# Performance work log

Measured on AMD Instinct MI355X. Metric: run time of the kernel, lower is better.

The kernel has to match this reference:

```python
import jax, jax.numpy as jnp
import numpy as np

N = 50000      # nodes
E = 800000     # edges
IN = 128       # in_feats
NH = 128       # n_hidden (per-head out_feats)
H = 2          # num_heads
P = 100000     # node pairs for the head MLP
C = 2          # n_classes
NEG_SLOPE = 0.2


def setup_inputs() -> dict:
    key = jax.random.key(0)
    ks = jax.random.split(key, 16)
    def glorot(k, shape, fan_in):
        return jax.random.normal(k, shape, jnp.float32) * (1.0 / np.sqrt(fan_in))
    return {
        "src": jax.random.randint(ks[0], (E,), 0, N),
        "dst": jax.random.randint(ks[1], (E,), 0, N),
        "h": jax.random.normal(ks[2], (N, IN), jnp.float32),
        "x1": jax.random.randint(ks[3], (P,), 0, N),
        "x2": jax.random.randint(ks[4], (P,), 0, N),
        # GATConv layer 0
        "W0": glorot(ks[5], (IN, H * NH), IN),
        "al0": glorot(ks[6], (H, NH), NH),
        "ar0": glorot(ks[7], (H, NH), NH),
        # GATConv layer 1
        "W1": glorot(ks[8], (NH, H * NH), NH),
        "al1": glorot(ks[9], (H, NH), NH),
        "ar1": glorot(ks[10], (H, NH), NH),
        # head MLP (weights stored as [in, out])
        "w1": glorot(ks[11], (3 * NH, NH), 3 * NH),
        "b1": jnp.zeros((NH,), jnp.float32),
        "w2": glorot(ks[12], (NH, C), NH),
        "b2": jnp.zeros((C,), jnp.float32),
    }


def gat_conv(h, src, dst, W, al, ar):
    # h: [N, d_in] -> feat: [N, H, F]
    feat = (h @ W).reshape(h.shape[0], H, -1)
    el = jnp.einsum("nhf,hf->nh", feat, al)  # [N, H]
    er = jnp.einsum("nhf,hf->nh", feat, ar)  # [N, H]
    e = jax.nn.leaky_relu(el[src] + er[dst], NEG_SLOPE)  # [E, H]
    # edge softmax segmented by destination node
    emax = jax.ops.segment_max(e, dst, num_segments=N)
    ee = jnp.exp(e - emax[dst])
    denom = jax.ops.segment_sum(ee, dst, num_segments=N)
    alpha = ee / (denom[dst] + 1e-9)                      # [E, H]
    msg = feat[src] * alpha[..., None]                    # [E, H, F]
    out = jax.ops.segment_sum(msg, dst, num_segments=N)   # [N, H, F]
    return jax.nn.relu(out)


def reference(src, dst, h, x1, x2, W0, al0, ar0, W1, al1, ar1, w1, b1, w2, b2):
    h = gat_conv(h, src, dst, W0, al0, ar0).mean(axis=1)  # [N, NH]
    h = gat_conv(h, src, dst, W1, al1, ar1).mean(axis=1)  # [N, NH]
    h1, h2 = h[x1], h[x2]                                 # [P, NH]
    z = jnp.concatenate([h1, h2, jnp.abs(h1 - h2)], axis=1)
    z = jax.nn.relu(z @ w1 + b1)
    return z @ w2 + b2                                    # [P, C]
```

## Files before the change

kernel.cpp:

```cpp
#include <hip/hip_runtime.h>
#include <hip/hip_bf16.h>

#define NN 50000
#define NE 800000
#define NPAIR 100000

typedef unsigned int u32;
typedef unsigned short u16;
typedef __attribute__((ext_vector_type(8))) short short8;
typedef __attribute__((ext_vector_type(4))) float f32x4;

__device__ __forceinline__ float bflo(u32 u) { return __uint_as_float(u << 16); }
__device__ __forceinline__ float bfhi(u32 u) { return __uint_as_float(u & 0xffff0000u); }
__device__ __forceinline__ u32 bfround(float f) {
    u32 u = __float_as_uint(f);
    return (u + 0x7fffu + ((u >> 16) & 1u)) >> 16;
}
__device__ __forceinline__ u32 packbf(float a, float b) {
    return bfround(a) | (bfround(b) << 16);
}

__global__ __launch_bounds__(256) void count_kernel(const int* __restrict__ dst, int* __restrict__ off) {
    int e = blockIdx.x * 256 + threadIdx.x;
    if (e < NE) atomicAdd(&off[dst[e] + 1], 1);
}

__global__ __launch_bounds__(256) void scan1(int* __restrict__ data, int* __restrict__ bsums, int n) {
    int tid = threadIdx.x;
    int i = blockIdx.x * 256 + tid;
    int v = (i < n) ? data[i] : 0;
    #pragma unroll
    for (int d = 1; d < 64; d <<= 1) {
        int t = __shfl_up(v, d);
        if ((tid & 63) >= d) v += t;
    }
    __shared__ int ws[4];
    if ((tid & 63) == 63) ws[tid >> 6] = v;
    __syncthreads();
    int w = tid >> 6;
    if (w > 0) v += ws[0];
    if (w > 1) v += ws[1];
    if (w > 2) v += ws[2];
    if (i < n) data[i] = v;
    if (tid == 255) bsums[blockIdx.x] = v;
}

__global__ __launch_bounds__(256) void scan2(int* __restrict__ bsums, int nb) {
    int tid = threadIdx.x;
    int v = (tid < nb) ? bsums[tid] : 0;
    #pragma unroll
    for (int d = 1; d < 64; d <<= 1) {
        int t = __shfl_up(v, d);
        if ((tid & 63) >= d) v += t;
    }
    __shared__ int ws[4];
    if ((tid & 63) == 63) ws[tid >> 6] = v;
    __syncthreads();
    int w = tid >> 6;
    if (w > 0) v += ws[0];
    if (w > 1) v += ws[1];
    if (w > 2) v += ws[2];
    if (tid < nb) bsums[tid] = v;
}

__global__ __launch_bounds__(256) void scan3(int* __restrict__ data, const int* __restrict__ bsums, int n) {
    int i = blockIdx.x * 256 + threadIdx.x;
    if (i < n && blockIdx.x > 0) data[i] += bsums[blockIdx.x - 1];
}

__global__ __launch_bounds__(256) void fill_kernel(const int* __restrict__ src, const int* __restrict__ dst,
                                                   const int* __restrict__ off,
                                                   int* __restrict__ cursor, int* __restrict__ srcs) {
    int e = blockIdx.x * 256 + threadIdx.x;
    if (e < NE) {
        int d = dst[e];
        int pos = off[d] + atomicAdd(&cursor[d], 1);
        srcs[pos] = src[e];
    }
}

__global__ __launch_bounds__(256) void pack_wg(const float* __restrict__ W, u16* __restrict__ Wp) {
    int id = blockIdx.x * 256 + threadIdx.x;
    if (id < 128 * 256) {
        int k = id >> 8, n = id & 255;
        int kt = k >> 5, kk = k & 31, lg = kk >> 3, j = kk & 7;
        int nt = n >> 4, ln = n & 15;
        int lane = lg * 16 + ln;
        Wp[(((kt * 16 + nt) * 64) + lane) * 8 + j] = (u16)bfround(W[id]);
    }
}

template<bool ABF16>
__global__ __launch_bounds__(256) void gemm_mfma(const void* __restrict__ Av,
                                                 const u16* __restrict__ Wp,
                                                 const float* __restrict__ al,
                                                 const float* __restrict__ ar,
                                                 u16* __restrict__ C,
                                                 float* __restrict__ att, int nrows) {
    __shared__ u16 sbuf[64 * 264];
    int rbase = blockIdx.x * 64;
    int tid = threadIdx.x;
    if (ABF16) {
        const uint4* A4 = (const uint4*)Av;
        for (int id = tid; id < 64 * 16; id += 256) {
            int r = id >> 4, seg = id & 15;
            int gr = rbase + r;
            uint4 v = make_uint4(0u, 0u, 0u, 0u);
            if (gr < nrows) v = A4[gr * 16 + seg];
            *(uint4*)&sbuf[r * 136 + seg * 8] = v;
        }
    } else {
        const float4* A4 = (const float4*)Av;
        for (int id = tid; id < 64 * 32; id += 256) {
            int r = id >> 5, seg = id & 31;
            int gr = rbase + r;
            float4 v = make_float4(0.f, 0.f, 0.f, 0.f);
            if (gr < nrows) v = A4[gr * 32 + seg];
            uint2 p;
            p.x = packbf(v.x, v.y);
            p.y = packbf(v.z, v.w);
            *(uint2*)&sbuf[r * 136 + seg * 4] = p;
        }
    }
    __syncthreads();
    int l = tid & 63, w = tid >> 6;
    int ln = l & 15, lg = l >> 4;
    f32x4 acc[16];
    #pragma unroll
    for (int nt = 0; nt < 16; ++nt) acc[nt] = (f32x4){0.f, 0.f, 0.f, 0.f};
    const short8* wp = (const short8*)Wp;
    const u16* arow = &sbuf[(w * 16 + ln) * 136 + lg * 8];
    #pragma unroll
    for (int kt = 0; kt < 4; ++kt) {
        short8 a = *(const short8*)&arow[kt * 32];
        #pragma unroll
        for (int nt = 0; nt < 16; ++nt) {
            short8 b = wp[(kt * 16 + nt) * 64 + l];
            acc[nt] = __builtin_amdgcn_mfma_f32_16x16x32_bf16(a, b, acc[nt], 0, 0, 0);
        }
    }
    float alv[16], arv[16];
    #pragma unroll
    for (int nt = 0; nt < 16; ++nt) {
        alv[nt] = al[nt * 16 + ln];
        arv[nt] = ar[nt * 16 + ln];
    }
    #pragma unroll
    for (int r = 0; r < 4; ++r) {
        float pl0 = 0.f, pr0 = 0.f, pl1 = 0.f, pr1 = 0.f;
        #pragma unroll
        for (int nt = 0; nt < 8; ++nt) {
            pl0 += acc[nt][r] * alv[nt];
            pr0 += acc[nt][r] * arv[nt];
            pl1 += acc[nt + 8][r] * alv[nt + 8];
            pr1 += acc[nt + 8][r] * arv[nt + 8];
        }
        #pragma unroll
        for (int m = 1; m < 16; m <<= 1) {
            pl0 += __shfl_xor(pl0, m); pr0 += __shfl_xor(pr0, m);
            pl1 += __shfl_xor(pl1, m); pr1 += __shfl_xor(pr1, m);
        }
        int grow = rbase + w * 16 + lg * 4 + r;
        if (ln == 0 && grow < nrows) {
            att[grow * 4 + 0] = pl0;
            att[grow * 4 + 1] = pl1;
            att[grow * 4 + 2] = pr0;
            att[grow * 4 + 3] = pr1;
        }
    }
    __syncthreads();
    #pragma unroll
    for (int nt = 0; nt < 16; ++nt) {
        int col = nt * 16 + ln;
        #pragma unroll
        for (int r = 0; r < 4; ++r) {
            int row = w * 16 + lg * 4 + r;
            sbuf[row * 264 + col] = (u16)bfround(acc[nt][r]);
        }
    }
    __syncthreads();
    uint4* C4 = (uint4*)C;
    for (int id = tid; id < 64 * 32; id += 256) {
        int r = id >> 5, seg = id & 31;
        int gr = rbase + r;
        if (gr < nrows) C4[gr * 32 + seg] = *(uint4*)&sbuf[r * 264 + seg * 8];
    }
}

__global__ __launch_bounds__(128) void aggregate(const u16* __restrict__ feat,
                                                 const int* __restrict__ off,
                                                 const int* __restrict__ srcs,
                                                 const float* __restrict__ att,
                                                 u16* __restrict__ hout) {
    int v = blockIdx.x;
    int s = off[v], e_end = off[v + 1];
    int deg = e_end - s;
    int tid = threadIdx.x;
    u32* houtu = (u32*)hout;
    const u32* featu = (const u32*)feat;
    if (deg == 0) {
        if (tid < 64) houtu[v * 64 + tid] = 0u;
        return;
    }
    const float4* att4 = (const float4*)att;
    float4 av = att4[v];
    float er0 = av.z, er1 = av.w;
    int h = tid >> 6;
    int wave = h;

    __shared__ int ush[256];
    __shared__ float w0sh[256], w1sh[256];
    __shared__ float red[2][4];
    __shared__ float dsh[2];
    __shared__ float2 osh[128];

    float accx = 0.f, accy = 0.f;
    const float* wh = h ? w1sh : w0sh;

    if (deg <= 256) {
        float e0a[2], e1a[2];
        float m0 = -1e30f, m1 = -1e30f;
        #pragma unroll
        for (int jj = 0; jj < 2; ++jj) {
            int j = tid + 128 * jj;
            e0a[jj] = -1e30f; e1a[jj] = -1e30f;
            if (j < deg) {
                int u = srcs[s + j];
                ush[j] = u;
                float4 au = att4[u];
                float a0 = au.x + er0; a0 = a0 > 0.f ? a0 : 0.2f * a0;
                float a1 = au.y + er1; a1 = a1 > 0.f ? a1 : 0.2f * a1;
                e0a[jj] = a0; e1a[jj] = a1;
                m0 = fmaxf(m0, a0); m1 = fmaxf(m1, a1);
            }
        }
        #pragma unroll
        for (int m = 1; m < 64; m <<= 1) {
            m0 = fmaxf(m0, __shfl_xor(m0, m));
            m1 = fmaxf(m1, __shfl_xor(m1, m));
        }
        if ((tid & 63) == 0) { red[wave][0] = m0; red[wave][1] = m1; }
        __syncthreads();
        m0 = fmaxf(red[0][0], red[1][0]);
        m1 = fmaxf(red[0][1], red[1][1]);
        float s0 = 0.f, s1 = 0.f;
        #pragma unroll
        for (int jj = 0; jj < 2; ++jj) {
            int j = tid + 128 * jj;
            if (j < deg) {
                float w0 = __expf(e0a[jj] - m0), w1 = __expf(e1a[jj] - m1);
                w0sh[j] = w0; w1sh[j] = w1;
                s0 += w0; s1 += w1;
            }
        }
        #pragma unroll
        for (int m = 1; m < 64; m <<= 1) { s0 += __shfl_xor(s0, m); s1 += __shfl_xor(s1, m); }
        if ((tid & 63) == 0) { red[wave][2] = s0; red[wave][3] = s1; }
        __syncthreads();
        if (tid == 0) {
            dsh[0] = red[0][2] + red[1][2];
            dsh[1] = red[0][3] + red[1][3];
        }
        __syncthreads();
        int k = 0;
        for (; k + 4 <= deg; k += 4) {
            int u0 = ush[k], u1 = ush[k + 1], u2 = ush[k + 2], u3 = ush[k + 3];
            float q0 = wh[k], q1 = wh[k + 1], q2 = wh[k + 2], q3 = wh[k + 3];
            u32 f0 = featu[u0 * 128 + tid];
            u32 f1 = featu[u1 * 128 + tid];
            u32 f2 = featu[u2 * 128 + tid];
            u32 f3 = featu[u3 * 128 + tid];
            accx += q0 * bflo(f0) + q1 * bflo(f1) + q2 * bflo(f2) + q3 * bflo(f3);
            accy += q0 * bfhi(f0) + q1 * bfhi(f1) + q2 * bfhi(f2) + q3 * bfhi(f3);
        }
        for (; k < deg; ++k) {
            u32 fu = featu[ush[k] * 128 + tid];
            accx += wh[k] * bflo(fu);
            accy += wh[k] * bfhi(fu);
        }
    } else {
        float m0 = -1e30f, m1 = -1e30f;
        for (int idx = s + tid; idx < e_end; idx += 128) {
            int u = srcs[idx];
            float4 au = att4[u];
            float a0 = au.x + er0; a0 = a0 > 0.f ? a0 : 0.2f * a0;
            float a1 = au.y + er1; a1 = a1 > 0.f ? a1 : 0.2f * a1;
            m0 = fmaxf(m0, a0); m1 = fmaxf(m1, a1);
        }
        #pragma unroll
        for (int m = 1; m < 64; m <<= 1) {
            m0 = fmaxf(m0, __shfl_xor(m0, m));
            m1 = fmaxf(m1, __shfl_xor(m1, m));
        }
        if ((tid & 63) == 0) { red[wave][0] = m0; red[wave][1] = m1; }
        __syncthreads();
        m0 = fmaxf(red[0][0], red[1][0]);
        m1 = fmaxf(red[0][1], red[1][1]);
        float dsum0 = 0.f, dsum1 = 0.f;
        for (int cb = 0; cb < deg; cb += 128) {
            int cn = min(128, deg - cb);
            __syncthreads();
            if (tid < cn) {
                int u = srcs[s + cb + tid];
                float4 au = att4[u];
                float a0 = au.x + er0; a0 = a0 > 0.f ? a0 : 0.2f * a0;
                float a1 = au.y + er1; a1 = a1 > 0.f ? a1 : 0.2f * a1;
                float w0 = __expf(a0 - m0), w1 = __expf(a1 - m1);
                w0sh[tid] = w0; w1sh[tid] = w1; ush[tid] = u;
                dsum0 += w0; dsum1 += w1;
            }
            __syncthreads();
            for (int k = 0; k < cn; ++k) {
                u32 fu = featu[ush[k] * 128 + tid];
                accx += wh[k] * bflo(fu);
                accy += wh[k] * bfhi(fu);
            }
        }
        #pragma unroll
        for (int m = 1; m < 64; m <<= 1) { dsum0 += __shfl_xor(dsum0, m); dsum1 += __shfl_xor(dsum1, m); }
        __syncthreads();
        if ((tid & 63) == 0) { red[wave][2] = dsum0; red[wave][3] = dsum1; }
        __syncthreads();
        if (tid == 0) {
            dsh[0] = red[0][2] + red[1][2];
            dsh[1] = red[0][3] + red[1][3];
        }
        __syncthreads();
    }
    float d = dsh[h] + 1e-9f;
    float ox = fmaxf(accx / d, 0.f);
    float oy = fmaxf(accy / d, 0.f);
    osh[tid] = make_float2(ox, oy);
    __syncthreads();
    if (tid < 64) {
        float2 a = osh[tid], b = osh[tid + 64];
        houtu[v * 64 + tid] = packbf(0.5f * (a.x + b.x), 0.5f * (a.y + b.y));
    }
}

__global__ __launch_bounds__(256) void pack_w1(const float* __restrict__ w1, u16* __restrict__ w1p) {
    int id = blockIdx.x * 256 + threadIdx.x;
    if (id < 384 * 128) {
        int k = id >> 7, n = id & 127;
        int kt = k >> 5, kk = k & 31, lg = kk >> 3, j = kk & 7;
        int ct = n >> 4, ln = n & 15;
        int lane = lg * 16 + ln;
        w1p[(((kt * 8 + ct) * 64) + lane) * 8 + j] = (u16)bfround(w1[id]);
    }
}

__global__ __launch_bounds__(256) void mlp_mfma(const u16* __restrict__ hf,
                                                const int* __restrict__ x1,
                                                const int* __restrict__ x2,
                                                const u16* __restrict__ w1p,
                                                const float* __restrict__ b1,
                                                const float* __restrict__ w2,
                                                const float* __restrict__ b2,
                                                float* __restrict__ out) {
    __shared__ u16 z[64][392];
    int pbase = blockIdx.x * 64;
    int tid = threadIdx.x;
    const uint4* hfu4 = (const uint4*)hf;
    for (int id = tid; id < 64 * 16; id += 256) {
        int p = id >> 4, seg = id & 15;
        int gp = pbase + p;
        uint4 v1 = make_uint4(0u, 0u, 0u, 0u), v2 = v1;
        if (gp < NPAIR) {
            v1 = hfu4[x1[gp] * 16 + seg];
            v2 = hfu4[x2[gp] * 16 + seg];
        }
        int c8 = seg << 3;
        *(uint4*)&z[p][c8] = v1;
        *(uint4*)&z[p][128 + c8] = v2;
        uint4 vd;
        vd.x = packbf(fabsf(bflo(v1.x) - bflo(v2.x)), fabsf(bfhi(v1.x) - bfhi(v2.x)));
        vd.y = packbf(fabsf(bflo(v1.y) - bflo(v2.y)), fabsf(bfhi(v1.y) - bfhi(v2.y)));
        vd.z = packbf(fabsf(bflo(v1.z) - bflo(v2.z)), fabsf(bfhi(v1.z) - bfhi(v2.z)));
        vd.w = packbf(fabsf(bflo(v1.w) - bflo(v2.w)), fabsf(bfhi(v1.w) - bfhi(v2.w)));
        *(uint4*)&z[p][256 + c8] = vd;
    }
    __syncthreads();
    int l = tid & 63, w = tid >> 6;
    int lg = l >> 4, ln = l & 15;
    f32x4 acc[8];
    #pragma unroll
    for (int ct = 0; ct < 8; ++ct) acc[ct] = (f32x4){0.f, 0.f, 0.f, 0.f};
    const short8* wp = (const short8*)w1p;
    const u16* zr = &z[w * 16 + ln][lg * 8];
    for (int kt = 0; kt < 12; ++kt) {
        short8 a = *(const short8*)&zr[kt * 32];
        #pragma unroll
        for (int ct = 0; ct < 8; ++ct) {
            short8 b = wp[(kt * 8 + ct) * 64 + l];
            acc[ct] = __builtin_amdgcn_mfma_f32_16x16x32_bf16(a, b, acc[ct], 0, 0, 0);
        }
    }
    float b1v[8], w20[8], w21[8];
    #pragma unroll
    for (int ct = 0; ct < 8; ++ct) {
        int n = ct * 16 + ln;
        b1v[ct] = b1[n];
        w20[ct] = w2[n * 2 + 0];
        w21[ct] = w2[n * 2 + 1];
    }
    float ob0 = b2[0], ob1 = b2[1];
    #pragma unroll
    for (int r = 0; r < 4; ++r) {
        float p0 = 0.f, p1 = 0.f;
        #pragma unroll
        for (int ct = 0; ct < 8; ++ct) {
            float zv = fmaxf(acc[ct][r] + b1v[ct], 0.f);
            p0 += zv * w20[ct]; p1 += zv * w21[ct];
        }
        #pragma unroll
        for (int m = 1; m < 16; m <<= 1) { p0 += __shfl_xor(p0, m); p1 += __shfl_xor(p1, m); }
        int gp = pbase + w * 16 + lg * 4 + r;
        if (ln == 0 && gp < NPAIR) {
            out[gp * 2 + 0] = p0 + ob0;
            out[gp * 2 + 1] = p1 + ob1;
        }
    }
}

extern "C" void kernel_launch(void* const* d_in, const int* in_sizes, int n_in,
                              void* d_out, int out_size, void* d_ws, size_t ws_size,
                              hipStream_t stream) {
    const int*   src = (const int*)d_in[0];
    const int*   dst = (const int*)d_in[1];
    const float* h   = (const float*)d_in[2];
    const int*   x1  = (const int*)d_in[3];
    const int*   x2  = (const int*)d_in[4];
    const float* W0  = (const float*)d_in[5];
    const float* al0 = (const float*)d_in[6];
    const float* ar0 = (const float*)d_in[7];
    const float* W1  = (const float*)d_in[8];
    const float* al1 = (const float*)d_in[9];
    const float* ar1 = (const float*)d_in[10];
    const float* w1  = (const float*)d_in[11];
    const float* b1  = (const float*)d_in[12];
    const float* w2  = (const float*)d_in[13];
    const float* b2  = (const float*)d_in[14];
    float* out = (float*)d_out;

    char* ws = (char*)d_ws;
    size_t o = 0;
    auto alloc = [&](size_t bytes) { size_t r = o; o = (o + bytes + 255) & ~255UL; return r; };
    int* off    = (int*)(ws + alloc((NN + 1) * sizeof(int)));
    int* cursor = (int*)(ws + alloc(NN * sizeof(int)));
    int* bsums  = (int*)(ws + alloc(256 * sizeof(int)));
    int* srcs   = (int*)(ws + alloc(NE * sizeof(int)));
    float* att  = (float*)(ws + alloc((size_t)NN * 4 * sizeof(float)));
    u16* feat   = (u16*)(ws + alloc((size_t)NN * 256 * sizeof(u16)));
    u16* hb0    = (u16*)(ws + alloc((size_t)NN * 128 * sizeof(u16)));
    u16* hb1    = (u16*)(ws + alloc((size_t)NN * 128 * sizeof(u16)));
    u16* w1p    = (u16*)(ws + alloc((size_t)384 * 128 * sizeof(u16)));
    u16* w0pg   = (u16*)(ws + alloc((size_t)128 * 256 * sizeof(u16)));
    u16* w1pg   = (u16*)(ws + alloc((size_t)128 * 256 * sizeof(u16)));

    hipMemsetAsync(off, 0, (NN + 1) * sizeof(int), stream);
    hipMemsetAsync(cursor, 0, NN * sizeof(int), stream);

    int eblocks = (NE + 255) / 256;
    int nscan = NN + 1;
    int nb = (nscan + 255) / 256;
    count_kernel<<<eblocks, 256, 0, stream>>>(dst, off);
    scan1<<<nb, 256, 0, stream>>>(off, bsums, nscan);
    scan2<<<1, 256, 0, stream>>>(bsums, nb);
    scan3<<<nb, 256, 0, stream>>>(off, bsums, nscan);
    fill_kernel<<<eblocks, 256, 0, stream>>>(src, dst, off, cursor, srcs);
    pack_wg<<<128, 256, 0, stream>>>(W0, w0pg);
    pack_wg<<<128, 256, 0, stream>>>(W1, w1pg);
    pack_w1<<<192, 256, 0, stream>>>(w1, w1p);

    int gblocks = (NN + 63) / 64;
    gemm_mfma<false><<<gblocks, 256, 0, stream>>>((const void*)h, w0pg, al0, ar0, feat, att, NN);
    aggregate<<<NN, 128, 0, stream>>>(feat, off, srcs, att, hb0);
    gemm_mfma<true><<<gblocks, 256, 0, stream>>>((const void*)hb0, w1pg, al1, ar1, feat, att, NN);
    aggregate<<<NN, 128, 0, stream>>>(feat, off, srcs, att, hb1);
    mlp_mfma<<<(NPAIR + 63) / 64, 256, 0, stream>>>(hb1, x1, x2, w1p, b1, w2, b2, out);
}
```

Measured before the change: 406.8 us.

## Aggregate one node per wavefront with online softmax and merge weight pack kernels

After: 383.2 us. 5.8% less time.

```diff
diff --git a/kernel.cpp b/kernel.cpp
--- a/kernel.cpp
+++ b/kernel.cpp
@@ -79,14 +79,27 @@
     }
 }
 
-__global__ __launch_bounds__(256) void pack_wg(const float* __restrict__ W, u16* __restrict__ Wp) {
+__global__ __launch_bounds__(256) void pack_all(const float* __restrict__ W0, const float* __restrict__ W1,
+                                                const float* __restrict__ w1,
+                                                u16* __restrict__ w0pg, u16* __restrict__ w1pg,
+                                                u16* __restrict__ w1p) {
     int id = blockIdx.x * 256 + threadIdx.x;
-    if (id < 128 * 256) {
-        int k = id >> 8, n = id & 255;
+    if (id < 65536) {
+        const float* W = (id < 32768) ? W0 : W1;
+        u16* Wp = (id < 32768) ? w0pg : w1pg;
+        int t = id & 32767;
+        int k = t >> 8, n = t & 255;
         int kt = k >> 5, kk = k & 31, lg = kk >> 3, j = kk & 7;
         int nt = n >> 4, ln = n & 15;
         int lane = lg * 16 + ln;
-        Wp[(((kt * 16 + nt) * 64) + lane) * 8 + j] = (u16)bfround(W[id]);
+        Wp[(((kt * 16 + nt) * 64) + lane) * 8 + j] = (u16)bfround(W[t]);
+    } else if (id < 65536 + 49152) {
+        int t = id - 65536;
+        int k = t >> 7, n = t & 127;
+        int kt = k >> 5, kk = k & 31, lg = kk >> 3, j = kk & 7;
+        int ct = n >> 4, ln = n & 15;
+        int lane = lg * 16 + ln;
+        w1p[(((kt * 8 + ct) * 64) + lane) * 8 + j] = (u16)bfround(w1[t]);
     }
 }
 
@@ -192,160 +205,89 @@
                                                  const int* __restrict__ srcs,
                                                  const float* __restrict__ att,
                                                  u16* __restrict__ hout) {
-    int v = blockIdx.x;
-    int s = off[v], e_end = off[v + 1];
-    int deg = e_end - s;
-    int tid = threadIdx.x;
-    u32* houtu = (u32*)hout;
-    const u32* featu = (const u32*)feat;
-    if (deg == 0) {
-        if (tid < 64) houtu[v * 64 + tid] = 0u;
-        return;
-    }
+    int v = blockIdx.x * 2 + (threadIdx.x >> 6);
+    int lane = threadIdx.x & 63;
+    if (v >= NN) return;
+    int s = off[v], deg = off[v + 1] - s;
     const float4* att4 = (const float4*)att;
+    const uint2* featu2 = (const uint2*)feat;
+    uint2* houtu2 = (uint2*)hout;
     float4 av = att4[v];
     float er0 = av.z, er1 = av.w;
-    int h = tid >> 6;
-    int wave = h;
-
-    __shared__ int ush[256];
-    __shared__ float w0sh[256], w1sh[256];
-    __shared__ float red[2][4];
-    __shared__ float dsh[2];
-    __shared__ float2 osh[128];
-
-    float accx = 0.f, accy = 0.f;
-    const float* wh = h ? w1sh : w0sh;
-
-    if (deg <= 256) {
-        float e0a[2], e1a[2];
-        float m0 = -1e30f, m1 = -1e30f;
-        #pragma unroll
-        for (int jj = 0; jj < 2; ++jj) {
-            int j = tid + 128 * jj;
-            e0a[jj] = -1e30f; e1a[jj] = -1e30f;
-            if (j < deg) {
-                int u = srcs[s + j];
-                ush[j] = u;
-                float4 au = att4[u];
-                float a0 = au.x + er0; a0 = a0 > 0.f ? a0 : 0.2f * a0;
-                float a1 = au.y + er1; a1 = a1 > 0.f ? a1 : 0.2f * a1;
-                e0a[jj] = a0; e1a[jj] = a1;
-                m0 = fmaxf(m0, a0); m1 = fmaxf(m1, a1);
-            }
-        }
-        #pragma unroll
-        for (int m = 1; m < 64; m <<= 1) {
-            m0 = fmaxf(m0, __shfl_xor(m0, m));
-            m1 = fmaxf(m1, __shfl_xor(m1, m));
-        }
-        if ((tid & 63) == 0) { red[wave][0] = m0; red[wave][1] = m1; }
-        __syncthreads();
-        m0 = fmaxf(red[0][0], red[1][0]);
-        m1 = fmaxf(red[0][1], red[1][1]);
-        float s0 = 0.f, s1 = 0.f;
-        #pragma unroll
-        for (int jj = 0; jj < 2; ++jj) {
-            int j = tid + 128 * jj;
-            if (j < deg) {
-                float w0 = __expf(e0a[jj] - m0), w1 = __expf(e1a[jj] - m1);
-                w0sh[j] = w0; w1sh[j] = w1;
-                s0 += w0; s1 += w1;
-            }
-        }
-        #pragma unroll
-        for (int m = 1; m < 64; m <<= 1) { s0 += __shfl_xor(s0, m); s1 += __shfl_xor(s1, m); }
-        if ((tid & 63) == 0) { red[wave][2] = s0; red[wave][3] = s1; }
-        __syncthreads();
-        if (tid == 0) {
-            dsh[0] = red[0][2] + red[1][2];
-            dsh[1] = red[0][3] + red[1][3];
-        }
-        __syncthreads();
-        int k = 0;
-        for (; k + 4 <= deg; k += 4) {
-            int u0 = ush[k], u1 = ush[k + 1], u2 = ush[k + 2], u3 = ush[k + 3];
-            float q0 = wh[k], q1 = wh[k + 1], q2 = wh[k + 2], q3 = wh[k + 3];
-            u32 f0 = featu[u0 * 128 + tid];
-            u32 f1 = featu[u1 * 128 + tid];
-            u32 f2 = featu[u2 * 128 + tid];
-            u32 f3 = featu[u3 * 128 + tid];
-            accx += q0 * bflo(f0) + q1 * bflo(f1) + q2 * bflo(f2) + q3 * bflo(f3);
-            accy += q0 * bfhi(f0) + q1 * bfhi(f1) + q2 * bfhi(f2) + q3 * bfhi(f3);
-        }
-        for (; k < deg; ++k) {
-            u32 fu = featu[ush[k] * 128 + tid];
-            accx += wh[k] * bflo(fu);
-            accy += wh[k] * bfhi(fu);
-        }
-    } else {
-        float m0 = -1e30f, m1 = -1e30f;
-        for (int idx = s + tid; idx < e_end; idx += 128) {
-            int u = srcs[idx];
+    bool h0 = lane < 32;
+    float m0 = -1e30f, m1 = -1e30f, d0 = 0.f, d1 = 0.f;
+    float a0 = 0.f, a1 = 0.f, a2 = 0.f, a3 = 0.f;
+    for (int cb = 0; cb < deg; cb += 64) {
+        int k = cb + lane;
+        int cn = min(64, deg - cb);
+        int u = 0;
+        float e0 = -1e30f, e1 = -1e30f;
+        if (k < deg) {
+            u = srcs[s + k];
             float4 au = att4[u];
-            float a0 = au.x + er0; a0 = a0 > 0.f ? a0 : 0.2f * a0;
-            float a1 = au.y + er1; a1 = a1 > 0.f ? a1 : 0.2f * a1;
-            m0 = fmaxf(m0, a0); m1 = fmaxf(m1, a1);
-        }
-        #pragma unroll
-        for (int m = 1; m < 64; m <<= 1) {
-            m0 = fmaxf(m0, __shfl_xor(m0, m));
-            m1 = fmaxf(m1, __shfl_xor(m1, m));
-        }
-        if ((tid & 63) == 0) { red[wave][0] = m0; red[wave][1] = m1; }
-        __syncthreads();
-        m0 = fmaxf(red[0][0], red[1][0]);
-        m1 = fmaxf(red[0][1], red[1][1]);
-        float dsum0 = 0.f, dsum1 = 0.f;
-        for (int cb = 0; cb < deg; cb += 128) {
-            int cn = min(128, deg - cb);
-            __syncthreads();
-            if (tid < cn) {
-                int u = srcs[s + cb + tid];
-                float4 au = att4[u];
-                float a0 = au.x + er0; a0 = a0 > 0.f ? a0 : 0.2f * a0;
-                float a1 = au.y + er1; a1 = a1 > 0.f ? a1 : 0.2f * a1;
-                float w0 = __expf(a0 - m0), w1 = __expf(a1 - m1);
-                w0sh[tid] = w0; w1sh[tid] = w1; ush[tid] = u;
-                dsum0 += w0; dsum1 += w1;
-            }
-            __syncthreads();
-            for (int k = 0; k < cn; ++k) {
-                u32 fu = featu[ush[k] * 128 + tid];
-                accx += wh[k] * bflo(fu);
-                accy += wh[k] * bfhi(fu);
-            }
-        }
-        #pragma unroll
-        for (int m = 1; m < 64; m <<= 1) { dsum0 += __shfl_xor(dsum0, m); dsum1 += __shfl_xor(dsum1, m); }
-        __syncthreads();
-        if ((tid & 63) == 0) { red[wave][2] = dsum0; red[wave][3] = dsum1; }
-        __syncthreads();
-        if (tid == 0) {
-            dsh[0] = red[0][2] + red[1][2];
-            dsh[1] = red[0][3] + red[1][3];
-        }
-        __syncthreads();
-    }
-    float d = dsh[h] + 1e-9f;
-    float ox = fmaxf(accx / d, 0.f);
-    float oy = fmaxf(accy / d, 0.f);
-    osh[tid] = make_float2(ox, oy);
-    __syncthreads();
-    if (tid < 64) {
-        float2 a = osh[tid], b = osh[tid + 64];
-        houtu[v * 64 + tid] = packbf(0.5f * (a.x + b.x), 0.5f * (a.y + b.y));
-    }
-}
-
-__global__ __launch_bounds__(256) void pack_w1(const float* __restrict__ w1, u16* __restrict__ w1p) {
-    int id = blockIdx.x * 256 + threadIdx.x;
-    if (id < 384 * 128) {
-        int k = id >> 7, n = id & 127;
-        int kt = k >> 5, kk = k & 31, lg = kk >> 3, j = kk & 7;
-        int ct = n >> 4, ln = n & 15;
-        int lane = lg * 16 + ln;
-        w1p[(((kt * 8 + ct) * 64) + lane) * 8 + j] = (u16)bfround(w1[id]);
+            e0 = au.x + er0; e0 = e0 > 0.f ? e0 : 0.2f * e0;
+            e1 = au.y + er1; e1 = e1 > 0.f ? e1 : 0.2f * e1;
+        }
+        float mc0 = e0, mc1 = e1;
+        #pragma unroll
+        for (int mm = 1; mm < 64; mm <<= 1) {
+            mc0 = fmaxf(mc0, __shfl_xor(mc0, mm));
+            mc1 = fmaxf(mc1, __shfl_xor(mc1, mm));
+        }
+        float m0n = fmaxf(m0, mc0), m1n = fmaxf(m1, mc1);
+        float f0 = __expf(m0 - m0n), f1 = __expf(m1 - m1n);
+        float w0 = (k < deg) ? __expf(e0 - m0n) : 0.f;
+        float w1 = (k < deg) ? __expf(e1 - m1n) : 0.f;
+        float s0 = w0, s1 = w1;
+        #pragma unroll
+        for (int mm = 1; mm < 64; mm <<= 1) {
+            s0 += __shfl_xor(s0, mm);
+            s1 += __shfl_xor(s1, mm);
+        }
+        d0 = d0 * f0 + s0;
+        d1 = d1 * f1 + s1;
+        float fa = h0 ? f0 : f1;
+        a0 *= fa; a1 *= fa; a2 *= fa; a3 *= fa;
+        m0 = m0n; m1 = m1n;
+        int k2 = 0;
+        for (; k2 + 4 <= cn; k2 += 4) {
+            int uu0 = __shfl(u, k2), uu1 = __shfl(u, k2 + 1);
+            int uu2 = __shfl(u, k2 + 2), uu3 = __shfl(u, k2 + 3);
+            float wa0 = __shfl(w0, k2), wb0 = __shfl(w1, k2);
+            float wa1 = __shfl(w0, k2 + 1), wb1 = __shfl(w1, k2 + 1);
+            float wa2 = __shfl(w0, k2 + 2), wb2 = __shfl(w1, k2 + 2);
+            float wa3 = __shfl(w0, k2 + 3), wb3 = __shfl(w1, k2 + 3);
+            float wk0 = h0 ? wa0 : wb0, wk1 = h0 ? wa1 : wb1;
+            float wk2 = h0 ? wa2 : wb2, wk3 = h0 ? wa3 : wb3;
+            uint2 g0 = featu2[(size_t)uu0 * 64 + lane];
+            uint2 g1 = featu2[(size_t)uu1 * 64 + lane];
+            uint2 g2 = featu2[(size_t)uu2 * 64 + lane];
+            uint2 g3 = featu2[(size_t)uu3 * 64 + lane];
+            a0 += wk0 * bflo(g0.x) + wk1 * bflo(g1.x) + wk2 * bflo(g2.x) + wk3 * bflo(g3.x);
+            a1 += wk0 * bfhi(g0.x) + wk1 * bfhi(g1.x) + wk2 * bfhi(g2.x) + wk3 * bfhi(g3.x);
+            a2 += wk0 * bflo(g0.y) + wk1 * bflo(g1.y) + wk2 * bflo(g2.y) + wk3 * bflo(g3.y);
+            a3 += wk0 * bfhi(g0.y) + wk1 * bfhi(g1.y) + wk2 * bfhi(g2.y) + wk3 * bfhi(g3.y);
+        }
+        for (; k2 < cn; ++k2) {
+            int uu = __shfl(u, k2);
+            float wa = __shfl(w0, k2), wb = __shfl(w1, k2);
+            float wk = h0 ? wa : wb;
+            uint2 g = featu2[(size_t)uu * 64 + lane];
+            a0 += wk * bflo(g.x); a1 += wk * bfhi(g.x);
+            a2 += wk * bflo(g.y); a3 += wk * bfhi(g.y);
+        }
+    }
+    float dh = h0 ? d0 : d1;
+    float r = 1.f / (dh + 1e-9f);
+    float o0 = fmaxf(a0 * r, 0.f), o1 = fmaxf(a1 * r, 0.f);
+    float o2 = fmaxf(a2 * r, 0.f), o3 = fmaxf(a3 * r, 0.f);
+    float p0 = __shfl_xor(o0, 32), p1 = __shfl_xor(o1, 32);
+    float p2 = __shfl_xor(o2, 32), p3 = __shfl_xor(o3, 32);
+    if (h0) {
+        uint2 q;
+        q.x = packbf(0.5f * (o0 + p0), 0.5f * (o1 + p1));
+        q.y = packbf(0.5f * (o2 + p2), 0.5f * (o3 + p3));
+        houtu2[(size_t)v * 32 + lane] = q;
     }
 }
 
@@ -468,14 +410,12 @@
     scan2<<<1, 256, 0, stream>>>(bsums, nb);
     scan3<<<nb, 256, 0, stream>>>(off, bsums, nscan);
     fill_kernel<<<eblocks, 256, 0, stream>>>(src, dst, off, cursor, srcs);
-    pack_wg<<<128, 256, 0, stream>>>(W0, w0pg);
-    pack_wg<<<128, 256, 0, stream>>>(W1, w1pg);
-    pack_w1<<<192, 256, 0, stream>>>(w1, w1p);
+    pack_all<<<448, 256, 0, stream>>>(W0, W1, w1, w0pg, w1pg, w1p);
 
     int gblocks = (NN + 63) / 64;
     gemm_mfma<false><<<gblocks, 256, 0, stream>>>((const void*)h, w0pg, al0, ar0, feat, att, NN);
-    aggregate<<<NN, 128, 0, stream>>>(feat, off, srcs, att, hb0);
+    aggregate<<<(NN + 1) / 2, 128, 0, stream>>>(feat, off, srcs, att, hb0);
     gemm_mfma<true><<<gblocks, 256, 0, stream>>>((const void*)hb0, w1pg, al1, ar1, feat, att, NN);
-    aggregate<<<NN, 128, 0, stream>>>(feat, off, srcs, att, hb1);
+    aggregate<<<(NN + 1) / 2, 128, 0, stream>>>(feat, off, srcs, att, hb1);
     mlp_mfma<<<(NPAIR + 63) / 64, 256, 0, stream>>>(hb1, x1, x2, w1p, b1, w2, b2, out);
 }
```
